# Kernel tuning notes

Hardware: AMD Instinct MI355X
Metric: run time of the kernel (lower is better)

Reference implementation:

```python
import jax, jax.numpy as jnp
import numpy as np

INPUT_DIMS = 512
OUTPUT_DIMS = 512
GRID_SIZE = 8


def setup_inputs() -> dict:
    key = jax.random.key(0)
    k_x, k_w = jax.random.split(key)
    x = jax.random.normal(k_x, (4, 2048, INPUT_DIMS), dtype=jnp.float32)
    scale = 1.0 / (np.sqrt(INPUT_DIMS) * np.sqrt(GRID_SIZE))
    fouriercoeffs = jax.random.normal(
        k_w, (2, OUTPUT_DIMS, INPUT_DIMS, GRID_SIZE), dtype=jnp.float32) * scale
    bias = jnp.zeros((1, OUTPUT_DIMS), dtype=jnp.float32)
    return {"x": x, "fouriercoeffs": fouriercoeffs, "bias": bias}


def reference(x, fouriercoeffs, bias):
    out_shape = x.shape[:-1] + (OUTPUT_DIMS,)
    xf = x.reshape(-1, INPUT_DIMS)  # [N, I]
    k = jnp.arange(1, GRID_SIZE + 1, dtype=x.dtype)  # [G]
    arg = xf[:, :, None] * k  # [N, I, G]
    # contract cos/sin features against coeffs: two batched GEMMs
    y = jnp.einsum('nig,oig->no', jnp.cos(arg), fouriercoeffs[0])
    y = y + jnp.einsum('nig,oig->no', jnp.sin(arg), fouriercoeffs[1])
    y = y + bias
    return y.reshape(out_shape)
```

## Files before the change

### kernel.cpp

```cpp
#include <hip/hip_runtime.h>
#include <hip/hip_bf16.h>


typedef __attribute__((ext_vector_type(8)))  short s16x8;
typedef __attribute__((ext_vector_type(4)))  int   i32x4;
typedef __attribute__((ext_vector_type(4)))  float f32x4;
typedef __attribute__((ext_vector_type(16))) float f32x16;

#define NROWS 8192
#define IDIM  512
#define ODIM  512
#define KDIM  8192

static __device__ __forceinline__ short f2bf(float f) {
    union { float f; unsigned u; } v; v.f = f;
    unsigned r = v.u + 0x7fffu + ((v.u >> 16) & 1u);
    return (short)(r >> 16);
}

static __device__ __forceinline__ float bf2f(short h) {
    union { unsigned u; float f; } v;
    v.u = ((unsigned)(unsigned short)h) << 16;
    return v.f;
}

static __device__ __forceinline__ int pkbf(float c, float s) {
    union { __hip_bfloat162 h; int i; } u;
    u.h = __float22bfloat162_rn(make_float2(c, s));
    return u.i;
}

__global__ __launch_bounds__(256) void fkan_prep(const float* __restrict__ cf,
                                                 short* __restrict__ Wb) {
    const int o = blockIdx.x;
    const int tid = threadIdx.x;
#pragma unroll
    for (int rep = 0; rep < 2; ++rep) {
        const int i = tid + rep * 256;
        const float* c0 = cf + (o * 512 + i) * 8;
        const float* c1 = cf + ((512 + o) * 512 + i) * 8;
        float4 a0 = *(const float4*)c0;
        float4 a1 = *(const float4*)(c0 + 4);
        float4 b0 = *(const float4*)c1;
        float4 b1 = *(const float4*)(c1 + 4);
        s16x8 lo, hi;
        lo[0] = f2bf(a0.x); lo[1] = f2bf(b0.x);
        lo[2] = f2bf(a0.y); lo[3] = f2bf(b0.y);
        lo[4] = f2bf(a0.z); lo[5] = f2bf(b0.z);
        lo[6] = f2bf(a0.w); lo[7] = f2bf(b0.w);
        hi[0] = f2bf(a1.x); hi[1] = f2bf(b1.x);
        hi[2] = f2bf(a1.y); hi[3] = f2bf(b1.y);
        hi[4] = f2bf(a1.z); hi[5] = f2bf(b1.z);
        hi[6] = f2bf(a1.w); hi[7] = f2bf(b1.w);
        *(s16x8*)(Wb + o * KDIM + i * 16)     = lo;
        *(s16x8*)(Wb + o * KDIM + i * 16 + 8) = hi;
    }
}

__global__ __launch_bounds__(512, 2) void fkan_gemm18(const float* __restrict__ x,
                                                      const short* __restrict__ Wb,
                                                      short* __restrict__ P) {
    __shared__ short As[2][256 * 72];
    __shared__ short Bs[2][256 * 64];

    const int bid = blockIdx.x;
    const int xcd = bid & 7;
    const int bn = xcd & 1, kc = xcd >> 1;
    const int bm = bid >> 3;
    const int n0 = bm * 256, o0 = bn * 256, i0 = kc * 128;
    const int kbase = i0 * 16;
    const int NKT = 32;

    const int tid = threadIdx.x;
    const int wid = tid >> 6, lane = tid & 63;
    const int l32 = lane & 31, hi32 = lane >> 5;
    const int wr = wid >> 2, wc = wid & 3;

    f32x16 acc[4][2];
#pragma unroll
    for (int a = 0; a < 4; ++a)
#pragma unroll
        for (int b = 0; b < 2; ++b)
#pragma unroll
            for (int e = 0; e < 16; ++e) acc[a][b][e] = 0.f;

    const int arow_s = tid >> 1, hsel = tid & 1;
    const float* xptr = x + (size_t)(n0 + arow_s) * 512 + i0 + 2 * hsel;

    auto stageB = [&](int t, int nb) {
#pragma unroll
        for (int w = 0; w < 4; ++w) {
            const int ch = w * 512 + tid;
            const int l = ch >> 3, sl = ch & 7;
            const int cb = sl ^ (l & 7);
            const short* src = Wb + (size_t)(o0 + l) * KDIM + kbase + t * 64 + cb * 8;
            short* ldst = &Bs[nb][w * 4096 + wid * 512];
            __builtin_amdgcn_global_load_lds(
                (const __attribute__((address_space(1))) void*)src,
                (__attribute__((address_space(3))) void*)ldst, 16, 0, 0);
        }
    };

    auto stageA = [&](int nb, float2 xv2) {
        short* Ab = As[nb];
#pragma unroll
        for (int j = 0; j < 2; ++j) {
            const float xx = j ? xv2.y : xv2.x;
            float s1, c1;
            __sincosf(xx, &s1, &c1);
            float c = c1, s = s1;
            i32x4 lo, hi;
#pragma unroll
            for (int g = 0; g < 8; ++g) {
                const int p = pkbf(c, s);
                if (g < 4) lo[g] = p; else hi[g - 4] = p;
                const float t1 = s * s1, t2 = c * s1;
                const float cn = __builtin_fmaf(c, c1, -t1);
                s = __builtin_fmaf(s, c1, t2);
                c = cn;
            }
            const int il = 2 * hsel + j;
            *(i32x4*)&Ab[arow_s * 72 + il * 16]     = lo;
            *(i32x4*)&Ab[arow_s * 72 + il * 16 + 8] = hi;
        }
    };

    float2 xv = *(const float2*)xptr;
    stageB(0, 0);
    stageA(0, xv);
    xv = *(const float2*)(xptr + 4);
    __syncthreads();

    for (int kt = 0; kt < NKT; ++kt) {
        const int cur = kt & 1;

        if (kt + 1 < NKT) stageB(kt + 1, cur ^ 1);

        s16x8 af[4][4], bfr[2][4];
#pragma unroll
        for (int mt = 0; mt < 4; ++mt)
#pragma unroll
            for (int kk = 0; kk < 4; ++kk) {
                const int row = wr * 128 + mt * 32 + l32;
                af[mt][kk] = *(const s16x8*)&As[cur][row * 72 + (kk * 2 + hi32) * 8];
            }
#pragma unroll
        for (int nt = 0; nt < 2; ++nt)
#pragma unroll
            for (int kk = 0; kk < 4; ++kk) {
                const int row = wc * 64 + nt * 32 + l32;
                const int cb = kk * 2 + hi32;
                bfr[nt][kk] = *(const s16x8*)&Bs[cur][row * 64 + (cb ^ (row & 7)) * 8];
            }

#pragma unroll
        for (int kk = 0; kk < 4; ++kk)
#pragma unroll
            for (int mt = 0; mt < 4; ++mt)
#pragma unroll
                for (int nt = 0; nt < 2; ++nt)
                    acc[mt][nt] = __builtin_amdgcn_mfma_f32_32x32x16_bf16(
                        af[mt][kk], bfr[nt][kk], acc[mt][nt], 0, 0, 0);

        if (kt + 1 < NKT) {
            stageA(cur ^ 1, xv);
            if (kt + 2 < NKT) xv = *(const float2*)(xptr + (kt + 2) * 4);
        }

        __syncthreads();
    }

    unsigned short* dst = (unsigned short*)P + (size_t)kc * (NROWS * ODIM);
#pragma unroll
    for (int mt = 0; mt < 4; ++mt)
#pragma unroll
        for (int nt = 0; nt < 2; ++nt) {
            const f32x16 v = acc[mt][nt];
            const int oc = o0 + wc * 64 + nt * 32 + l32;
            const int rb = n0 + wr * 128 + mt * 32 + 4 * hi32;
#pragma unroll
            for (int reg = 0; reg < 16; ++reg) {
                const int row = rb + (reg & 3) + 8 * (reg >> 2);
                dst[(size_t)row * 512 + oc] = (unsigned short)f2bf(v[reg]);
            }
        }
}

__global__ __launch_bounds__(256) void fkan_combine4(const short* __restrict__ P,
                                                     const float* __restrict__ bias,
                                                     float* __restrict__ out) {
    const int total = NROWS * ODIM;
    const int stride = gridDim.x * 256 * 8;
    for (int e = (blockIdx.x * 256 + threadIdx.x) * 8; e < total; e += stride) {
        s16x8 a = *(const s16x8*)(P + e);
        s16x8 b = *(const s16x8*)(P + total + e);
        s16x8 c = *(const s16x8*)(P + 2 * total + e);
        s16x8 d = *(const s16x8*)(P + 3 * total + e);
        const int col = e & 511;
        float4 c0 = *(const float4*)(bias + col);
        float4 c1 = *(const float4*)(bias + col + 4);
        float4 r0, r1;
        r0.x = (bf2f(a[0]) + bf2f(b[0])) + (bf2f(c[0]) + bf2f(d[0])) + c0.x;
        r0.y = (bf2f(a[1]) + bf2f(b[1])) + (bf2f(c[1]) + bf2f(d[1])) + c0.y;
        r0.z = (bf2f(a[2]) + bf2f(b[2])) + (bf2f(c[2]) + bf2f(d[2])) + c0.z;
        r0.w = (bf2f(a[3]) + bf2f(b[3])) + (bf2f(c[3]) + bf2f(d[3])) + c0.w;
        r1.x = (bf2f(a[4]) + bf2f(b[4])) + (bf2f(c[4]) + bf2f(d[4])) + c1.x;
        r1.y = (bf2f(a[5]) + bf2f(b[5])) + (bf2f(c[5]) + bf2f(d[5])) + c1.y;
        r1.z = (bf2f(a[6]) + bf2f(b[6])) + (bf2f(c[6]) + bf2f(d[6])) + c1.z;
        r1.w = (bf2f(a[7]) + bf2f(b[7])) + (bf2f(c[7]) + bf2f(d[7])) + c1.w;
        *(float4*)(out + e)     = r0;
        *(float4*)(out + e + 4) = r1;
    }
}

__global__ __launch_bounds__(256, 2) void fkan_gemm_fb(const float* __restrict__ x,
                                                       const short* __restrict__ Wb,
                                                       const float* __restrict__ bias,
                                                       float* __restrict__ outp) {
    __shared__ short As[2][128 * 64];
    __shared__ short Bs[2][128 * 64];
    const int bid = blockIdx.x;
    const int xcd = bid & 7, idx = bid >> 3;
    const int bn = xcd & 3, bm = idx + (xcd >> 2) * 32;
    const int n0 = bm * 128, o0 = bn * 128;
    const int tid = threadIdx.x;
    const int wid = tid >> 6, lane = tid & 63;
    const int lrow = lane & 15, lk = lane >> 4;
    const int wr = wid >> 1, wc = wid & 1;
    f32x4 acc[4][4];
#pragma unroll
    for (int a = 0; a < 4; ++a)
#pragma unroll
        for (int b = 0; b < 4; ++b) { f32x4 z = {0,0,0,0}; acc[a][b] = z; }
    const int nl = tid >> 1, isel = tid & 1;
    const float* xrow = x + (n0 + nl) * 512 + isel * 2;
    auto stage = [&](int t, int nb, float2 xvv) {
#pragma unroll
        for (int w = 0; w < 4; ++w) {
            const int chunk = w * 256 + tid;
            const int r = chunk >> 3, pc = chunk & 7;
            const int lc = pc ^ (r & 7);
            const short* src = Wb + (o0 + r) * KDIM + t * 64 + lc * 8;
            short* ldst = &Bs[nb][w * 2048 + wid * 512];
            __builtin_amdgcn_global_load_lds(
                (const __attribute__((address_space(1))) void*)src,
                (__attribute__((address_space(3))) void*)ldst, 16, 0, 0);
        }
#pragma unroll
        for (int ii = 0; ii < 2; ++ii) {
            const float xx = ii ? xvv.y : xvv.x;
            float s1, c1; __sincosf(xx, &s1, &c1);
            float c = c1, s = s1;
            i32x4 lo, hi;
#pragma unroll
            for (int g = 0; g < 8; ++g) {
                const int p = pkbf(c, s);
                if (g < 4) lo[g] = p; else hi[g - 4] = p;
                const float t1 = s * s1, t2 = c * s1;
                const float cn = __builtin_fmaf(c, c1, -t1);
                s = __builtin_fmaf(s, c1, t2); c = cn;
            }
            const int cb0 = (isel * 2 + ii) * 2;
            *(i32x4*)&As[nb][nl * 64 + ((cb0 ^ (nl & 7))) * 8]       = lo;
            *(i32x4*)&As[nb][nl * 64 + (((cb0 + 1) ^ (nl & 7))) * 8] = hi;
        }
    };
    float2 xv = *(const float2*)xrow;
    stage(0, 0, xv);
    xv = *(const float2*)(xrow + 4);
    __syncthreads();
    for (int kt = 0; kt < 128; ++kt) {
        const int cur = kt & 1;
        s16x8 af[2][4], bfr[2][4];
#pragma unroll
        for (int ksub = 0; ksub < 2; ++ksub) {
#pragma unroll
            for (int mf = 0; mf < 4; ++mf) {
                const int row = wr * 64 + mf * 16 + lrow;
                af[ksub][mf] = *(const s16x8*)&As[cur][row * 64 + ((ksub * 4 + lk) ^ (row & 7)) * 8];
            }
#pragma unroll
            for (int nf = 0; nf < 4; ++nf) {
                const int row = wc * 64 + nf * 16 + lrow;
                bfr[ksub][nf] = *(const s16x8*)&Bs[cur][row * 64 + ((ksub * 4 + lk) ^ (row & 7)) * 8];
            }
        }
        if (kt + 1 < 128) {
            stage(kt + 1, cur ^ 1, xv);
            if (kt + 2 < 128) xv = *(const float2*)(xrow + (kt + 2) * 4);
        }
#pragma unroll
        for (int ksub = 0; ksub < 2; ++ksub)
#pragma unroll
            for (int mf = 0; mf < 4; ++mf)
#pragma unroll
                for (int nf = 0; nf < 4; ++nf)
                    acc[mf][nf] = __builtin_amdgcn_mfma_f32_16x16x32_bf16(
                        af[ksub][mf], bfr[ksub][nf], acc[mf][nf], 0, 0, 0);
        __syncthreads();
    }
#pragma unroll
    for (int nf = 0; nf < 4; ++nf) {
        const int oc = o0 + wc * 64 + nf * 16 + lrow;
        const float bv = bias[oc];
#pragma unroll
        for (int mf = 0; mf < 4; ++mf) {
            const f32x4 v = acc[mf][nf];
            const int rbase = n0 + wr * 64 + mf * 16 + lk * 4;
#pragma unroll
            for (int j = 0; j < 4; ++j)
                outp[(size_t)(rbase + j) * 512 + oc] = v[j] + bv;
        }
    }
}

extern "C" void kernel_launch(void* const* d_in, const int* in_sizes, int n_in,
                              void* d_out, int out_size, void* d_ws, size_t ws_size,
                              hipStream_t stream) {
    const float* x    = (const float*)d_in[0];
    const float* cf   = (const float*)d_in[1];
    const float* bias = (const float*)d_in[2];
    float* out = (float*)d_out;

    const size_t partial_bytes = (size_t)4 * NROWS * ODIM * 2;
    const size_t wb_bytes = (size_t)ODIM * KDIM * 2;

    if (ws_size >= partial_bytes + wb_bytes) {
        short* P  = (short*)d_ws;
        short* Wb = (short*)((char*)d_ws + partial_bytes);
        fkan_prep<<<512, 256, 0, stream>>>(cf, Wb);
        fkan_gemm18<<<256, 512, 0, stream>>>(x, Wb, P);
        fkan_combine4<<<2048, 256, 0, stream>>>(P, bias, out);
    } else {
        short* Wb = (short*)d_ws;
        fkan_prep<<<512, 256, 0, stream>>>(cf, Wb);
        fkan_gemm_fb<<<256, 256, 0, stream>>>(x, Wb, bias, out);
    }
}
```

Before: 88.76 us.

## Build A fragments in registers with permlane swap instead of LDS staging

Drops the shared-memory A tile and has each wave compute its cos/sin bf16 fragments directly from x in registers, using v_permlane32_swap to rearrange them into the MFMA operand layout. This removes the LDS writes and reads for A and halves LDS usage. In exchange, each A row's trig features are recomputed by every column-wave, multiplying the sincos/rotation ALU work, and register pressure rises.

Measured after the change: 147.5 us. 66.2% more time.

```diff
diff --git a/kernel.cpp b/kernel.cpp
--- a/kernel.cpp
+++ b/kernel.cpp
@@ -57,10 +57,9 @@
     }
 }
 
-__global__ __launch_bounds__(512, 2) void fkan_gemm18(const float* __restrict__ x,
+__global__ __launch_bounds__(512, 2) void fkan_gemm19(const float* __restrict__ x,
                                                       const short* __restrict__ Wb,
                                                       short* __restrict__ P) {
-    __shared__ short As[2][256 * 72];
     __shared__ short Bs[2][256 * 64];
 
     const int bid = blockIdx.x;
@@ -84,8 +83,10 @@
 #pragma unroll
             for (int e = 0; e < 16; ++e) acc[a][b][e] = 0.f;
 
-    const int arow_s = tid >> 1, hsel = tid & 1;
-    const float* xptr = x + (size_t)(n0 + arow_s) * 512 + i0 + 2 * hsel;
+    const float* xr[4];
+#pragma unroll
+    for (int mt = 0; mt < 4; ++mt)
+        xr[mt] = x + (size_t)(n0 + wr * 128 + mt * 32 + l32) * 512 + i0;
 
     auto stageB = [&](int t, int nb) {
 #pragma unroll
@@ -101,49 +102,40 @@
         }
     };
 
-    auto stageA = [&](int nb, float2 xv2) {
-        short* Ab = As[nb];
-#pragma unroll
-        for (int j = 0; j < 2; ++j) {
-            const float xx = j ? xv2.y : xv2.x;
-            float s1, c1;
-            __sincosf(xx, &s1, &c1);
-            float c = c1, s = s1;
-            i32x4 lo, hi;
-#pragma unroll
-            for (int g = 0; g < 8; ++g) {
-                const int p = pkbf(c, s);
-                if (g < 4) lo[g] = p; else hi[g - 4] = p;
-                const float t1 = s * s1, t2 = c * s1;
-                const float cn = __builtin_fmaf(c, c1, -t1);
-                s = __builtin_fmaf(s, c1, t2);
-                c = cn;
-            }
-            const int il = 2 * hsel + j;
-            *(i32x4*)&Ab[arow_s * 72 + il * 16]     = lo;
-            *(i32x4*)&Ab[arow_s * 72 + il * 16 + 8] = hi;
-        }
+    auto buildA2 = [&](float xx, s16x8& f0, s16x8& f1) {
+        float s1, c1;
+        __sincosf(xx, &s1, &c1);
+        float c = c1, s = s1;
+        int I[8];
+#pragma unroll
+        for (int g = 0; g < 8; ++g) {
+            I[g] = pkbf(c, s);
+            const float t1 = s * s1, t2 = c * s1;
+            const float cn = __builtin_fmaf(c, c1, -t1);
+            s = __builtin_fmaf(s, c1, t2);
+            c = cn;
+        }
+        i32x4 a0, a1;
+#pragma unroll
+        for (int g = 0; g < 4; ++g) {
+            int va = I[g], vb = I[g + 4];
+            asm volatile("v_permlane32_swap_b32 %0, %1" : "+v"(va), "+v"(vb));
+            a0[g] = va; a1[g] = vb;
+        }
+        f0 = *(s16x8*)&a0;
+        f1 = *(s16x8*)&a1;
     };
 
-    float2 xv = *(const float2*)xptr;
+    float4 xq[4];
     stageB(0, 0);
-    stageA(0, xv);
-    xv = *(const float2*)(xptr + 4);
+#pragma unroll
+    for (int mt = 0; mt < 4; ++mt) xq[mt] = *(const float4*)(xr[mt]);
     __syncthreads();
 
     for (int kt = 0; kt < NKT; ++kt) {
         const int cur = kt & 1;
 
-        if (kt + 1 < NKT) stageB(kt + 1, cur ^ 1);
-
-        s16x8 af[4][4], bfr[2][4];
-#pragma unroll
-        for (int mt = 0; mt < 4; ++mt)
-#pragma unroll
-            for (int kk = 0; kk < 4; ++kk) {
-                const int row = wr * 128 + mt * 32 + l32;
-                af[mt][kk] = *(const s16x8*)&As[cur][row * 72 + (kk * 2 + hi32) * 8];
-            }
+        s16x8 bfr[2][4];
 #pragma unroll
         for (int nt = 0; nt < 2; ++nt)
 #pragma unroll
@@ -153,19 +145,31 @@
                 bfr[nt][kk] = *(const s16x8*)&Bs[cur][row * 64 + (cb ^ (row & 7)) * 8];
             }
 
-#pragma unroll
-        for (int kk = 0; kk < 4; ++kk)
+        float4 xn[4];
+        if (kt + 1 < NKT) {
+            stageB(kt + 1, cur ^ 1);
 #pragma unroll
             for (int mt = 0; mt < 4; ++mt)
+                xn[mt] = *(const float4*)(xr[mt] + (kt + 1) * 4);
+        }
+
+#pragma unroll
+        for (int mt = 0; mt < 4; ++mt) {
+            const float xx0 = hi32 ? xq[mt].y : xq[mt].x;
+            const float xx1 = hi32 ? xq[mt].w : xq[mt].z;
+            s16x8 af[4];
+            buildA2(xx0, af[0], af[1]);
+            buildA2(xx1, af[2], af[3]);
+#pragma unroll
+            for (int kk = 0; kk < 4; ++kk)
 #pragma unroll
                 for (int nt = 0; nt < 2; ++nt)
                     acc[mt][nt] = __builtin_amdgcn_mfma_f32_32x32x16_bf16(
-                        af[mt][kk], bfr[nt][kk], acc[mt][nt], 0, 0, 0);
-
-        if (kt + 1 < NKT) {
-            stageA(cur ^ 1, xv);
-            if (kt + 2 < NKT) xv = *(const float2*)(xptr + (kt + 2) * 4);
-        }
+                        af[kk], bfr[nt][kk], acc[mt][nt], 0, 0, 0);
+        }
+
+#pragma unroll
+        for (int mt = 0; mt < 4; ++mt) xq[mt] = xn[mt];
 
         __syncthreads();
     }
@@ -329,7 +333,7 @@
         short* P  = (short*)d_ws;
         short* Wb = (short*)((char*)d_ws + partial_bytes);
         fkan_prep<<<512, 256, 0, stream>>>(cf, Wb);
-        fkan_gemm18<<<256, 512, 0, stream>>>(x, Wb, P);
+        fkan_gemm19<<<256, 512, 0, stream>>>(x, Wb, P);
         fkan_combine4<<<2048, 256, 0, stream>>>(P, bias, out);
     } else {
         short* Wb = (short*)d_ws;
```
